# Optimization experiments

Measured on AMD Instinct MI355X. Metric: run time of the kernel, lower is better.

The kernel has to match this reference:

```python
import jax, jax.numpy as jnp
import numpy as np

N_NODES = 100000


def gcn_conv(x, edge_index, W, b):
    """PyG-style GCNConv: symmetric-normalized A+I propagation of x @ W, plus bias."""
    n = x.shape[0]
    src, dst = edge_index[0], edge_index[1]
    loops = jnp.arange(n, dtype=src.dtype)
    src = jnp.concatenate([src, loops])  # add self loops
    dst = jnp.concatenate([dst, loops])
    deg = jax.ops.segment_sum(jnp.ones_like(src, dtype=x.dtype), dst, num_segments=n)
    dinv = jnp.where(deg > 0, jax.lax.rsqrt(deg), 0.0)
    norm = dinv[src] * dinv[dst]  # [E+n]
    h = x @ W  # [n, out]
    msg = h[src] * norm[:, None]  # gather + scale
    out = jax.ops.segment_sum(msg, dst, num_segments=n)  # scatter-add
    return out + b


def setup_inputs() -> dict:
    key = jax.random.key(0)
    ks = jax.random.split(key, 5)
    x = jax.random.normal(ks[0], (N_NODES, 4), dtype=jnp.float32)
    edge_index = jax.random.randint(ks[1], (2, 3200000), 0, N_NODES, dtype=jnp.int64)
    W1 = jax.random.normal(ks[2], (4, 64), dtype=jnp.float32) * 0.5
    b1 = jnp.zeros((64,), dtype=jnp.float32)
    W2 = jax.random.normal(ks[3], (64, 32), dtype=jnp.float32) * 0.125
    b2 = jnp.zeros((32,), dtype=jnp.float32)
    return {"x": x, "edge_index": edge_index, "W1": W1, "b1": b1, "W2": W2, "b2": b2}


def reference(x, edge_index, W1, b1, W2, b2):
    h = gcn_conv(x, edge_index, W1, b1)
    h = jax.nn.relu(h)
    # F.dropout with training=False is identity (eval-mode reference)
    h = gcn_conv(h, edge_index, W2, b2)
    return jnp.mean(h, axis=0)  # [32]
```

## Files before the change

### kernel.cpp

```cpp
#include <hip/hip_runtime.h>

#define ST 512
#define EPB 8192
#define CT 1024
#define FT 1024
#define S_LOG 8
#define S 256
#define CAP 8912
#define MAXB 512

__device__ __forceinline__ void gAtomAdd(float* p, float v) {
    unsafeAtomicAdd(p, v);
}

__global__ void k_init(int* __restrict__ cur_d, int* __restrict__ cur_s,
                       float* __restrict__ g, int nb) {
    int t = threadIdx.x;
    if (t < nb) { cur_d[t] = t * CAP; cur_s[t] = t * CAP; }
    if (t < 64) g[t] = 0.0f;
}

__global__ void __launch_bounds__(ST) k_sctr2(
        const int4* __restrict__ src4, const int4* __restrict__ dst4, int E,
        int* __restrict__ cur_d, int* __restrict__ cur_s,
        unsigned* __restrict__ rec_d, unsigned* __restrict__ rec_s, int nb) {
    __shared__ unsigned lrec[EPB];
    __shared__ unsigned short lbkt[EPB];
    __shared__ int cnt[MAXB];
    __shared__ int lst[MAXB];
    __shared__ int gb[MAXB];
    int t = threadIdx.x;
    int E4 = E >> 2;
    int b4 = blockIdx.x * (EPB / 4);
    int m = min(EPB, E - blockIdx.x * EPB);

    int4 dk[4], sk[4];
    bool v[4];
    #pragma unroll
    for (int k = 0; k < 4; ++k) {
        int idx = b4 + k * ST + t;
        v[k] = idx < E4;
        if (v[k]) { dk[k] = dst4[idx]; sk[k] = src4[idx]; }
    }

    for (int ph = 0; ph < 2; ++ph) {
        int* cursor = ph ? cur_s : cur_d;
        unsigned* rec = ph ? rec_s : rec_d;
        cnt[t] = 0;
        __syncthreads();
        int rk[16];
        #pragma unroll
        for (int k = 0; k < 4; ++k) {
            if (v[k]) {
                int4 K = ph ? sk[k] : dk[k];
                rk[4 * k + 0] = atomicAdd(&cnt[K.x >> S_LOG], 1);
                rk[4 * k + 1] = atomicAdd(&cnt[K.y >> S_LOG], 1);
                rk[4 * k + 2] = atomicAdd(&cnt[K.z >> S_LOG], 1);
                rk[4 * k + 3] = atomicAdd(&cnt[K.w >> S_LOG], 1);
            }
        }
        __syncthreads();
        int c = cnt[t];
        for (int o = 1; o < MAXB; o <<= 1) {
            int u = (t >= o) ? cnt[t - o] : 0;
            __syncthreads();
            cnt[t] += u;
            __syncthreads();
        }
        lst[t] = cnt[t] - c;
        gb[t] = (c > 0) ? atomicAdd(&cursor[t], c) : 0;
        __syncthreads();
        #pragma unroll
        for (int k = 0; k < 4; ++k) {
            if (v[k]) {
                int4 K = ph ? sk[k] : dk[k];
                int4 P = ph ? dk[k] : sk[k];
                int bb, p;
                bb = K.x >> S_LOG; p = lst[bb] + rk[4 * k + 0];
                lrec[p] = ((unsigned)P.x << S_LOG) | (unsigned)(K.x & (S - 1));
                lbkt[p] = (unsigned short)bb;
                bb = K.y >> S_LOG; p = lst[bb] + rk[4 * k + 1];
                lrec[p] = ((unsigned)P.y << S_LOG) | (unsigned)(K.y & (S - 1));
                lbkt[p] = (unsigned short)bb;
                bb = K.z >> S_LOG; p = lst[bb] + rk[4 * k + 2];
                lrec[p] = ((unsigned)P.z << S_LOG) | (unsigned)(K.z & (S - 1));
                lbkt[p] = (unsigned short)bb;
                bb = K.w >> S_LOG; p = lst[bb] + rk[4 * k + 3];
                lrec[p] = ((unsigned)P.w << S_LOG) | (unsigned)(K.w & (S - 1));
                lbkt[p] = (unsigned short)bb;
            }
        }
        __syncthreads();
        for (int i = t; i < m; i += ST) {
            int bb = lbkt[i];
            rec[gb[bb] + (i - lst[bb])] = lrec[i];
        }
        __syncthreads();
    }
}

__global__ void __launch_bounds__(CT) k_csry(
        unsigned* __restrict__ rec, const int* __restrict__ cur_d,
        const float4* __restrict__ x, float* __restrict__ dinv,
        float4* __restrict__ y, int* __restrict__ nst_g, int* __restrict__ nend_g,
        int n) {
    __shared__ unsigned lrec[CAP];
    __shared__ int cnt[S];
    __shared__ int nst[S];
    int b = blockIdx.x, t = threadIdx.x;
    int lo = b * CAP;
    int m = cur_d[b] - lo;
    if (t < S) cnt[t] = 0;
    __syncthreads();
    unsigned rv[9]; int rr[9];
    #pragma unroll
    for (int k = 0; k < 9; ++k) {
        int i = t + k * CT;
        if (i < m) {
            unsigned r = rec[lo + i];
            rv[k] = r;
            rr[k] = atomicAdd(&cnt[r & (S - 1)], 1);
        }
    }
    __syncthreads();
    int deg = (t < S) ? cnt[t] : 0;
    int nd = (b << S_LOG) + t;
    if (t < S && nd < n) {
        float dv = rsqrtf((float)deg + 1.0f);
        dinv[nd] = dv;
        float4 xi = x[nd];
        y[nd] = make_float4(dv * xi.x, dv * xi.y, dv * xi.z, dv * xi.w);
    }
    for (int o = 1; o < S; o <<= 1) {
        int u = (t < S && t >= o) ? cnt[t - o] : 0;
        __syncthreads();
        if (t < S) cnt[t] += u;
        __syncthreads();
    }
    if (t < S) {
        int st = cnt[t] - deg;
        nst[t] = st;
        if (nd < n) { nst_g[nd] = lo + st; nend_g[nd] = lo + st + deg; }
    }
    __syncthreads();
    #pragma unroll
    for (int k = 0; k < 9; ++k) {
        int i = t + k * CT;
        if (i < m) lrec[nst[rv[k] & (S - 1)] + rr[k]] = rv[k] >> S_LOG;
    }
    __syncthreads();
    for (int i = t; i < m; i += CT) rec[lo + i] = lrec[i];
}

__global__ void __launch_bounds__(FT) k_fuse(
        const unsigned* __restrict__ rec_d, const unsigned* __restrict__ rec_s,
        const int* __restrict__ cur_s, const int* __restrict__ nst_g,
        const int* __restrict__ nend_g, const float4* __restrict__ y,
        const float* __restrict__ dinv,
        const float* __restrict__ W1, const float* __restrict__ b1,
        float* __restrict__ g, int n) {
    __shared__ float a[S];
    __shared__ float4 lp1[S];
    __shared__ float red[FT];
    int b = blockIdx.x, t = threadIdx.x;
    if (t < S) a[t] = 0.0f;
    __syncthreads();
    int lo = b * CAP;
    int m = cur_s[b] - lo;
    int m4 = m >> 2;
    const uint4* rec4 = (const uint4*)(rec_s + lo);
    for (int i = t; i < m4; i += FT) {
        uint4 r = rec4[i];
        float d0 = dinv[r.x >> S_LOG], d1 = dinv[r.y >> S_LOG];
        float d2 = dinv[r.z >> S_LOG], d3 = dinv[r.w >> S_LOG];
        atomicAdd(&a[r.x & (S - 1)], d0);
        atomicAdd(&a[r.y & (S - 1)], d1);
        atomicAdd(&a[r.z & (S - 1)], d2);
        atomicAdd(&a[r.w & (S - 1)], d3);
    }
    for (int i = (m4 << 2) + t; i < m; i += FT) {
        unsigned r = rec_s[lo + i];
        atomicAdd(&a[r & (S - 1)], dinv[r >> S_LOG]);
    }
    int node = t >> 2, q = t & 3;
    int nd = (b << S_LOG) + node;
    if (nd < n) {
        int j1 = nend_g[nd];
        int j = nst_g[nd] + q;
        float a0 = 0.0f, a1 = 0.0f, a2 = 0.0f, a3 = 0.0f;
        for (; j + 28 < j1; j += 32) {
            int s0 = rec_d[j],      s1 = rec_d[j + 4],  s2 = rec_d[j + 8],  s3 = rec_d[j + 12];
            int s4 = rec_d[j + 16], s5 = rec_d[j + 20], s6 = rec_d[j + 24], s7 = rec_d[j + 28];
            float4 y0 = y[s0], y1 = y[s1], y2 = y[s2], y3 = y[s3];
            float4 y4 = y[s4], y5 = y[s5], y6 = y[s6], y7 = y[s7];
            a0 += (y0.x + y1.x) + (y2.x + y3.x) + (y4.x + y5.x) + (y6.x + y7.x);
            a1 += (y0.y + y1.y) + (y2.y + y3.y) + (y4.y + y5.y) + (y6.y + y7.y);
            a2 += (y0.z + y1.z) + (y2.z + y3.z) + (y4.z + y5.z) + (y6.z + y7.z);
            a3 += (y0.w + y1.w) + (y2.w + y3.w) + (y4.w + y5.w) + (y6.w + y7.w);
        }
        for (; j + 12 < j1; j += 16) {
            int s0 = rec_d[j], s1 = rec_d[j + 4], s2 = rec_d[j + 8], s3 = rec_d[j + 12];
            float4 y0 = y[s0], y1 = y[s1], y2 = y[s2], y3 = y[s3];
            a0 += (y0.x + y1.x) + (y2.x + y3.x);
            a1 += (y0.y + y1.y) + (y2.y + y3.y);
            a2 += (y0.z + y1.z) + (y2.z + y3.z);
            a3 += (y0.w + y1.w) + (y2.w + y3.w);
        }
        for (; j < j1; j += 4) {
            float4 ys = y[rec_d[j]];
            a0 += ys.x; a1 += ys.y; a2 += ys.z; a3 += ys.w;
        }
        a0 += __shfl_down(a0, 2); a1 += __shfl_down(a1, 2);
        a2 += __shfl_down(a2, 2); a3 += __shfl_down(a3, 2);
        a0 += __shfl_down(a0, 1); a1 += __shfl_down(a1, 1);
        a2 += __shfl_down(a2, 1); a3 += __shfl_down(a3, 1);
        if (q == 0) {
            float di = dinv[nd];
            lp1[node] = make_float4(di * a0, di * a1, di * a2, di * a3);
        }
    }
    __syncthreads();
    int c = t & 63, w = t >> 6;
    float w0 = W1[c], w1 = W1[64 + c], w2 = W1[128 + c], w3 = W1[192 + c];
    float bb = b1[c];
    int nb0 = b << S_LOG;
    float facc = 0.0f;
    for (int k = w; k < S; k += 16) {
        int ndk = nb0 + k;
        if (ndk >= n) break;
        float di = dinv[ndk];
        float4 p = lp1[k];
        float4 yi = y[ndk];
        float h0 = fmaf(di, yi.x, p.x);
        float h1 = fmaf(di, yi.y, p.y);
        float h2 = fmaf(di, yi.z, p.z);
        float h3 = fmaf(di, yi.w, p.w);
        float h = fmaf(h0, w0, fmaf(h1, w1, fmaf(h2, w2, fmaf(h3, w3, bb))));
        h = fmaxf(h, 0.0f);
        float wi = fmaf(di, a[k], di * di);
        facc = fmaf(wi, h, facc);
    }
    red[t] = facc;
    __syncthreads();
    if (t < 64) {
        float s = red[t];
        #pragma unroll
        for (int o = 1; o < 16; ++o) s += red[t + 64 * o];
        gAtomAdd(&g[t], s);
    }
}

__global__ void k_final(const float* __restrict__ g, const float* __restrict__ W2,
                        const float* __restrict__ b2, float* __restrict__ out, float inv_n) {
    int j = threadIdx.x;
    if (j < 32) {
        float a = 0.0f;
        #pragma unroll
        for (int c = 0; c < 64; ++c) a = fmaf(g[c], W2[c * 32 + j], a);
        out[j] = fmaf(a, inv_n, b2[j]);
    }
}

extern "C" void kernel_launch(void* const* d_in, const int* in_sizes, int n_in,
                              void* d_out, int out_size, void* d_ws, size_t ws_size,
                              hipStream_t stream) {
    const float* x  = (const float*)d_in[0];
    const int*   ei = (const int*)d_in[1];
    const float* W1 = (const float*)d_in[2];
    const float* b1 = (const float*)d_in[3];
    const float* W2 = (const float*)d_in[4];
    const float* b2 = (const float*)d_in[5];
    float* out = (float*)d_out;

    int n = in_sizes[0] / 4;
    int E = in_sizes[1] / 2;
    const int* src = ei;
    const int* dst = ei + E;
    int NB = (n + S - 1) >> S_LOG;

    char* ws = (char*)d_ws;
    int* cur_d = (int*)ws;
    int* cur_s = cur_d + 512;
    float* g   = (float*)(cur_s + 512);
    size_t ctrl = 1600;
    unsigned* rec_d = (unsigned*)ws + ctrl;
    unsigned* rec_s = rec_d + (size_t)NB * CAP;
    float* y    = (float*)(rec_s + (size_t)NB * CAP);
    float* dinv = y + 4 * (size_t)n;
    int* nst_g  = (int*)(dinv + (size_t)n);
    int* nend_g = nst_g + (size_t)n;

    int NSB = (E + EPB - 1) / EPB;

    k_init<<<1, 512, 0, stream>>>(cur_d, cur_s, g, NB);
    k_sctr2<<<NSB, ST, 0, stream>>>((const int4*)src, (const int4*)dst, E,
                                    cur_d, cur_s, rec_d, rec_s, NB);
    k_csry<<<NB, CT, 0, stream>>>(rec_d, cur_d, (const float4*)x, dinv,
                                  (float4*)y, nst_g, nend_g, n);
    k_fuse<<<NB, FT, 0, stream>>>(rec_d, rec_s, cur_s, nst_g, nend_g,
                                  (const float4*)y, dinv, W1, b1, g, n);
    k_final<<<1, 64, 0, stream>>>(g, W2, b2, out, 1.0f / (float)n);
}
```

Before: 156.9 us.

## Split scatter phases across blocks and keep per-bucket CSR sort in shared memory

The two-phase bucket scatter now runs as twice as many blocks, one phase each, instead of looping over both phases inside every block. The CSR local sort is moved out of the degree kernel. A lighter k_dy kernel only counts degrees and writes dinv and y. The merged aggregation kernel rebuilds the sorted neighbour list in shared memory and gathers from there, so the sorted records are no longer written back to global memory and nst/nend arrays are no longer needed. The cost is a second pass over rec_d for counting, and a larger shared-memory footprint in the merged kernel, which may lower occupancy.

```diff
diff --git a/kernel.cpp b/kernel.cpp
--- a/kernel.cpp
+++ b/kernel.cpp
@@ -2,8 +2,8 @@
 
 #define ST 512
 #define EPB 8192
-#define CT 1024
-#define FT 1024
+#define DT 512
+#define MT 1024
 #define S_LOG 8
 #define S 256
 #define CAP 8912
@@ -20,8 +20,8 @@
     if (t < 64) g[t] = 0.0f;
 }
 
-__global__ void __launch_bounds__(ST) k_sctr2(
-        const int4* __restrict__ src4, const int4* __restrict__ dst4, int E,
+__global__ void __launch_bounds__(ST) k_sctr1(
+        const int4* __restrict__ src4, const int4* __restrict__ dst4, int E, int NSB,
         int* __restrict__ cur_d, int* __restrict__ cur_s,
         unsigned* __restrict__ rec_d, unsigned* __restrict__ rec_s, int nb) {
     __shared__ unsigned lrec[EPB];
@@ -30,167 +30,174 @@
     __shared__ int lst[MAXB];
     __shared__ int gb[MAXB];
     int t = threadIdx.x;
+    int ph = blockIdx.x >= NSB;
+    int bid = ph ? blockIdx.x - NSB : blockIdx.x;
+    const int4* key4 = ph ? src4 : dst4;
+    const int4* pay4 = ph ? dst4 : src4;
+    int* cursor = ph ? cur_s : cur_d;
+    unsigned* rec = ph ? rec_s : rec_d;
     int E4 = E >> 2;
-    int b4 = blockIdx.x * (EPB / 4);
-    int m = min(EPB, E - blockIdx.x * EPB);
-
-    int4 dk[4], sk[4];
+    int b4 = bid * (EPB / 4);
+    int m = min(EPB, E - bid * EPB);
+
+    cnt[t] = 0;
+    __syncthreads();
+    int4 K[4], P[4];
     bool v[4];
+    int rk[16];
     #pragma unroll
     for (int k = 0; k < 4; ++k) {
         int idx = b4 + k * ST + t;
         v[k] = idx < E4;
-        if (v[k]) { dk[k] = dst4[idx]; sk[k] = src4[idx]; }
-    }
-
-    for (int ph = 0; ph < 2; ++ph) {
-        int* cursor = ph ? cur_s : cur_d;
-        unsigned* rec = ph ? rec_s : rec_d;
-        cnt[t] = 0;
+        if (v[k]) { K[k] = key4[idx]; P[k] = pay4[idx]; }
+    }
+    #pragma unroll
+    for (int k = 0; k < 4; ++k) {
+        if (v[k]) {
+            rk[4 * k + 0] = atomicAdd(&cnt[K[k].x >> S_LOG], 1);
+            rk[4 * k + 1] = atomicAdd(&cnt[K[k].y >> S_LOG], 1);
+            rk[4 * k + 2] = atomicAdd(&cnt[K[k].z >> S_LOG], 1);
+            rk[4 * k + 3] = atomicAdd(&cnt[K[k].w >> S_LOG], 1);
+        }
+    }
+    __syncthreads();
+    int c = cnt[t];
+    for (int o = 1; o < MAXB; o <<= 1) {
+        int u = (t >= o) ? cnt[t - o] : 0;
         __syncthreads();
-        int rk[16];
-        #pragma unroll
-        for (int k = 0; k < 4; ++k) {
-            if (v[k]) {
-                int4 K = ph ? sk[k] : dk[k];
-                rk[4 * k + 0] = atomicAdd(&cnt[K.x >> S_LOG], 1);
-                rk[4 * k + 1] = atomicAdd(&cnt[K.y >> S_LOG], 1);
-                rk[4 * k + 2] = atomicAdd(&cnt[K.z >> S_LOG], 1);
-                rk[4 * k + 3] = atomicAdd(&cnt[K.w >> S_LOG], 1);
-            }
-        }
+        cnt[t] += u;
         __syncthreads();
-        int c = cnt[t];
-        for (int o = 1; o < MAXB; o <<= 1) {
-            int u = (t >= o) ? cnt[t - o] : 0;
-            __syncthreads();
-            cnt[t] += u;
-            __syncthreads();
-        }
-        lst[t] = cnt[t] - c;
-        gb[t] = (c > 0) ? atomicAdd(&cursor[t], c) : 0;
-        __syncthreads();
-        #pragma unroll
-        for (int k = 0; k < 4; ++k) {
-            if (v[k]) {
-                int4 K = ph ? sk[k] : dk[k];
-                int4 P = ph ? dk[k] : sk[k];
-                int bb, p;
-                bb = K.x >> S_LOG; p = lst[bb] + rk[4 * k + 0];
-                lrec[p] = ((unsigned)P.x << S_LOG) | (unsigned)(K.x & (S - 1));
-                lbkt[p] = (unsigned short)bb;
-                bb = K.y >> S_LOG; p = lst[bb] + rk[4 * k + 1];
-                lrec[p] = ((unsigned)P.y << S_LOG) | (unsigned)(K.y & (S - 1));
-                lbkt[p] = (unsigned short)bb;
-                bb = K.z >> S_LOG; p = lst[bb] + rk[4 * k + 2];
-                lrec[p] = ((unsigned)P.z << S_LOG) | (unsigned)(K.z & (S - 1));
-                lbkt[p] = (unsigned short)bb;
-                bb = K.w >> S_LOG; p = lst[bb] + rk[4 * k + 3];
-                lrec[p] = ((unsigned)P.w << S_LOG) | (unsigned)(K.w & (S - 1));
-                lbkt[p] = (unsigned short)bb;
-            }
-        }
-        __syncthreads();
-        for (int i = t; i < m; i += ST) {
-            int bb = lbkt[i];
-            rec[gb[bb] + (i - lst[bb])] = lrec[i];
-        }
-        __syncthreads();
-    }
-}
-
-__global__ void __launch_bounds__(CT) k_csry(
-        unsigned* __restrict__ rec, const int* __restrict__ cur_d,
+    }
+    lst[t] = cnt[t] - c;
+    gb[t] = (c > 0) ? atomicAdd(&cursor[t], c) : 0;
+    __syncthreads();
+    #pragma unroll
+    for (int k = 0; k < 4; ++k) {
+        if (v[k]) {
+            int bb, p;
+            bb = K[k].x >> S_LOG; p = lst[bb] + rk[4 * k + 0];
+            lrec[p] = ((unsigned)P[k].x << S_LOG) | (unsigned)(K[k].x & (S - 1));
+            lbkt[p] = (unsigned short)bb;
+            bb = K[k].y >> S_LOG; p = lst[bb] + rk[4 * k + 1];
+            lrec[p] = ((unsigned)P[k].y << S_LOG) | (unsigned)(K[k].y & (S - 1));
+            lbkt[p] = (unsigned short)bb;
+            bb = K[k].z >> S_LOG; p = lst[bb] + rk[4 * k + 2];
+            lrec[p] = ((unsigned)P[k].z << S_LOG) | (unsigned)(K[k].z & (S - 1));
+            lbkt[p] = (unsigned short)bb;
+            bb = K[k].w >> S_LOG; p = lst[bb] + rk[4 * k + 3];
+            lrec[p] = ((unsigned)P[k].w << S_LOG) | (unsigned)(K[k].w & (S - 1));
+            lbkt[p] = (unsigned short)bb;
+        }
+    }
+    __syncthreads();
+    for (int i = t; i < m; i += ST) {
+        int bb = lbkt[i];
+        rec[gb[bb] + (i - lst[bb])] = lrec[i];
+    }
+}
+
+__global__ void __launch_bounds__(DT) k_dy(
+        const unsigned* __restrict__ rec_d, const int* __restrict__ cur_d,
         const float4* __restrict__ x, float* __restrict__ dinv,
-        float4* __restrict__ y, int* __restrict__ nst_g, int* __restrict__ nend_g,
-        int n) {
-    __shared__ unsigned lrec[CAP];
+        float4* __restrict__ y, int n) {
     __shared__ int cnt[S];
-    __shared__ int nst[S];
     int b = blockIdx.x, t = threadIdx.x;
     int lo = b * CAP;
-    int m = cur_d[b] - lo;
+    int md = cur_d[b] - lo;
     if (t < S) cnt[t] = 0;
     __syncthreads();
+    int m4 = md >> 2;
+    const uint4* r4 = (const uint4*)(rec_d + lo);
+    for (int i = t; i < m4; i += DT) {
+        uint4 r = r4[i];
+        atomicAdd(&cnt[r.x & (S - 1)], 1);
+        atomicAdd(&cnt[r.y & (S - 1)], 1);
+        atomicAdd(&cnt[r.z & (S - 1)], 1);
+        atomicAdd(&cnt[r.w & (S - 1)], 1);
+    }
+    for (int i = (m4 << 2) + t; i < md; i += DT)
+        atomicAdd(&cnt[rec_d[lo + i] & (S - 1)], 1);
+    __syncthreads();
+    if (t < S) {
+        int nd = (b << S_LOG) + t;
+        if (nd < n) {
+            float dv = rsqrtf((float)cnt[t] + 1.0f);
+            dinv[nd] = dv;
+            float4 xi = x[nd];
+            y[nd] = make_float4(dv * xi.x, dv * xi.y, dv * xi.z, dv * xi.w);
+        }
+    }
+}
+
+__global__ void __launch_bounds__(MT) k_mrg(
+        const unsigned* __restrict__ rec_d, const unsigned* __restrict__ rec_s,
+        const int* __restrict__ cur_d, const int* __restrict__ cur_s,
+        const float4* __restrict__ y, const float* __restrict__ dinv,
+        const float* __restrict__ W1, const float* __restrict__ b1,
+        float* __restrict__ g, int n) {
+    __shared__ unsigned lrec[CAP];
+    __shared__ int cnt[S], nst[S];
+    __shared__ float sd[S];
+    __shared__ float4 lp1[S];
+    __shared__ float red[MT];
+    int b = blockIdx.x, t = threadIdx.x;
+    int lo = b * CAP;
+    int md = cur_d[b] - lo;
+    if (t < S) { cnt[t] = 0; sd[t] = 0.0f; }
+    __syncthreads();
     unsigned rv[9]; int rr[9];
     #pragma unroll
     for (int k = 0; k < 9; ++k) {
-        int i = t + k * CT;
-        if (i < m) {
-            unsigned r = rec[lo + i];
+        int i = t + k * MT;
+        if (i < md) {
+            unsigned r = rec_d[lo + i];
             rv[k] = r;
             rr[k] = atomicAdd(&cnt[r & (S - 1)], 1);
         }
     }
     __syncthreads();
     int deg = (t < S) ? cnt[t] : 0;
-    int nd = (b << S_LOG) + t;
-    if (t < S && nd < n) {
-        float dv = rsqrtf((float)deg + 1.0f);
-        dinv[nd] = dv;
-        float4 xi = x[nd];
-        y[nd] = make_float4(dv * xi.x, dv * xi.y, dv * xi.z, dv * xi.w);
-    }
     for (int o = 1; o < S; o <<= 1) {
         int u = (t < S && t >= o) ? cnt[t - o] : 0;
         __syncthreads();
         if (t < S) cnt[t] += u;
         __syncthreads();
     }
-    if (t < S) {
-        int st = cnt[t] - deg;
-        nst[t] = st;
-        if (nd < n) { nst_g[nd] = lo + st; nend_g[nd] = lo + st + deg; }
-    }
+    if (t < S) nst[t] = cnt[t] - deg;
     __syncthreads();
     #pragma unroll
     for (int k = 0; k < 9; ++k) {
-        int i = t + k * CT;
-        if (i < m) lrec[nst[rv[k] & (S - 1)] + rr[k]] = rv[k] >> S_LOG;
-    }
-    __syncthreads();
-    for (int i = t; i < m; i += CT) rec[lo + i] = lrec[i];
-}
-
-__global__ void __launch_bounds__(FT) k_fuse(
-        const unsigned* __restrict__ rec_d, const unsigned* __restrict__ rec_s,
-        const int* __restrict__ cur_s, const int* __restrict__ nst_g,
-        const int* __restrict__ nend_g, const float4* __restrict__ y,
-        const float* __restrict__ dinv,
-        const float* __restrict__ W1, const float* __restrict__ b1,
-        float* __restrict__ g, int n) {
-    __shared__ float a[S];
-    __shared__ float4 lp1[S];
-    __shared__ float red[FT];
-    int b = blockIdx.x, t = threadIdx.x;
-    if (t < S) a[t] = 0.0f;
-    __syncthreads();
-    int lo = b * CAP;
-    int m = cur_s[b] - lo;
-    int m4 = m >> 2;
-    const uint4* rec4 = (const uint4*)(rec_s + lo);
-    for (int i = t; i < m4; i += FT) {
-        uint4 r = rec4[i];
-        float d0 = dinv[r.x >> S_LOG], d1 = dinv[r.y >> S_LOG];
-        float d2 = dinv[r.z >> S_LOG], d3 = dinv[r.w >> S_LOG];
-        atomicAdd(&a[r.x & (S - 1)], d0);
-        atomicAdd(&a[r.y & (S - 1)], d1);
-        atomicAdd(&a[r.z & (S - 1)], d2);
-        atomicAdd(&a[r.w & (S - 1)], d3);
-    }
-    for (int i = (m4 << 2) + t; i < m; i += FT) {
-        unsigned r = rec_s[lo + i];
-        atomicAdd(&a[r & (S - 1)], dinv[r >> S_LOG]);
-    }
+        int i = t + k * MT;
+        if (i < md) lrec[nst[rv[k] & (S - 1)] + rr[k]] = rv[k] >> S_LOG;
+    }
+    {
+        int ms = cur_s[b] - lo;
+        int m4 = ms >> 2;
+        const uint4* r4 = (const uint4*)(rec_s + lo);
+        for (int i = t; i < m4; i += MT) {
+            uint4 r = r4[i];
+            float d0 = dinv[r.x >> S_LOG], d1 = dinv[r.y >> S_LOG];
+            float d2 = dinv[r.z >> S_LOG], d3 = dinv[r.w >> S_LOG];
+            atomicAdd(&sd[r.x & (S - 1)], d0);
+            atomicAdd(&sd[r.y & (S - 1)], d1);
+            atomicAdd(&sd[r.z & (S - 1)], d2);
+            atomicAdd(&sd[r.w & (S - 1)], d3);
+        }
+        for (int i = (m4 << 2) + t; i < ms; i += MT) {
+            unsigned r = rec_s[lo + i];
+            atomicAdd(&sd[r & (S - 1)], dinv[r >> S_LOG]);
+        }
+    }
+    __syncthreads();
     int node = t >> 2, q = t & 3;
     int nd = (b << S_LOG) + node;
     if (nd < n) {
-        int j1 = nend_g[nd];
-        int j = nst_g[nd] + q;
+        int j = nst[node] + q;
+        int j1 = cnt[node];
         float a0 = 0.0f, a1 = 0.0f, a2 = 0.0f, a3 = 0.0f;
         for (; j + 28 < j1; j += 32) {
-            int s0 = rec_d[j],      s1 = rec_d[j + 4],  s2 = rec_d[j + 8],  s3 = rec_d[j + 12];
-            int s4 = rec_d[j + 16], s5 = rec_d[j + 20], s6 = rec_d[j + 24], s7 = rec_d[j + 28];
+            int s0 = lrec[j],      s1 = lrec[j + 4],  s2 = lrec[j + 8],  s3 = lrec[j + 12];
+            int s4 = lrec[j + 16], s5 = lrec[j + 20], s6 = lrec[j + 24], s7 = lrec[j + 28];
             float4 y0 = y[s0], y1 = y[s1], y2 = y[s2], y3 = y[s3];
             float4 y4 = y[s4], y5 = y[s5], y6 = y[s6], y7 = y[s7];
             a0 += (y0.x + y1.x) + (y2.x + y3.x) + (y4.x + y5.x) + (y6.x + y7.x);
@@ -199,7 +206,7 @@
             a3 += (y0.w + y1.w) + (y2.w + y3.w) + (y4.w + y5.w) + (y6.w + y7.w);
         }
         for (; j + 12 < j1; j += 16) {
-            int s0 = rec_d[j], s1 = rec_d[j + 4], s2 = rec_d[j + 8], s3 = rec_d[j + 12];
+            int s0 = lrec[j], s1 = lrec[j + 4], s2 = lrec[j + 8], s3 = lrec[j + 12];
             float4 y0 = y[s0], y1 = y[s1], y2 = y[s2], y3 = y[s3];
             a0 += (y0.x + y1.x) + (y2.x + y3.x);
             a1 += (y0.y + y1.y) + (y2.y + y3.y);
@@ -207,7 +214,7 @@
             a3 += (y0.w + y1.w) + (y2.w + y3.w);
         }
         for (; j < j1; j += 4) {
-            float4 ys = y[rec_d[j]];
+            float4 ys = y[lrec[j]];
             a0 += ys.x; a1 += ys.y; a2 += ys.z; a3 += ys.w;
         }
         a0 += __shfl_down(a0, 2); a1 += __shfl_down(a1, 2);
@@ -237,7 +244,7 @@
         float h3 = fmaf(di, yi.w, p.w);
         float h = fmaf(h0, w0, fmaf(h1, w1, fmaf(h2, w2, fmaf(h3, w3, bb))));
         h = fmaxf(h, 0.0f);
-        float wi = fmaf(di, a[k], di * di);
+        float wi = fmaf(di, sd[k], di * di);
         facc = fmaf(wi, h, facc);
     }
     red[t] = facc;
@@ -285,19 +292,17 @@
     size_t ctrl = 1600;
     unsigned* rec_d = (unsigned*)ws + ctrl;
     unsigned* rec_s = rec_d + (size_t)NB * CAP;
-    float* y    = (float*)(rec_s + (size_t)NB * CAP);
-    float* dinv = y + 4 * (size_t)n;
-    int* nst_g  = (int*)(dinv + (size_t)n);
-    int* nend_g = nst_g + (size_t)n;
+    float* yv   = (float*)(rec_s + (size_t)NB * CAP);
+    float* dinv = yv + 4 * (size_t)n;
 
     int NSB = (E + EPB - 1) / EPB;
 
     k_init<<<1, 512, 0, stream>>>(cur_d, cur_s, g, NB);
-    k_sctr2<<<NSB, ST, 0, stream>>>((const int4*)src, (const int4*)dst, E,
-                                    cur_d, cur_s, rec_d, rec_s, NB);
-    k_csry<<<NB, CT, 0, stream>>>(rec_d, cur_d, (const float4*)x, dinv,
-                                  (float4*)y, nst_g, nend_g, n);
-    k_fuse<<<NB, FT, 0, stream>>>(rec_d, rec_s, cur_s, nst_g, nend_g,
-                                  (const float4*)y, dinv, W1, b1, g, n);
+    k_sctr1<<<2 * NSB, ST, 0, stream>>>((const int4*)src, (const int4*)dst, E, NSB,
+                                        cur_d, cur_s, rec_d, rec_s, NB);
+    k_dy<<<NB, DT, 0, stream>>>(rec_d, cur_d, (const float4*)x, dinv,
+                                (float4*)yv, n);
+    k_mrg<<<NB, MT, 0, stream>>>(rec_d, rec_s, cur_d, cur_s,
+                                 (const float4*)yv, dinv, W1, b1, g, n);
     k_final<<<1, 64, 0, stream>>>(g, W2, b2, out, 1.0f / (float)n);
 }
```

New measurement: 155.1 us. No clear change (-1.1%).
